# Optimization experiments

Measured on AMD Instinct MI355X. Metric: run time of the kernel, lower is better.

Reference implementation:

```python
import jax, jax.numpy as jnp
import numpy as np

HIDDEN = 2048
HEAD_DIM = 128
NUM_HEADS = 8
NUM_HH = 2          # num_householder
CONV = 4
EPS = 1e-5
KEY_DIM = NUM_HEADS * HEAD_DIM  # 1024


def setup_inputs() -> dict:
    key = jax.random.key(0)
    ks = jax.random.split(key, 14)
    B, L = 2, 512
    s = 0.02
    x = jax.random.normal(ks[0], (B, L, HIDDEN), jnp.float32)
    Wq = jax.random.normal(ks[1], (HIDDEN, KEY_DIM), jnp.float32) * s
    Wk = jax.random.normal(ks[2], (HIDDEN, KEY_DIM * NUM_HH), jnp.float32) * s
    Wv = jax.random.normal(ks[3], (HIDDEN, KEY_DIM * NUM_HH), jnp.float32) * s
    Wb = jax.random.normal(ks[4], (HIDDEN, NUM_HEADS * NUM_HH), jnp.float32) * s
    Wa = jax.random.normal(ks[5], (HIDDEN, NUM_HEADS), jnp.float32) * s
    A_log = jnp.log(jax.random.uniform(ks[6], (NUM_HEADS,), jnp.float32, 1e-3, 16.0))
    dt = jnp.exp(jax.random.uniform(ks[7], (NUM_HEADS,), jnp.float32)
                 * (np.float32(np.log(0.1)) - np.float32(np.log(0.001)))
                 + np.float32(np.log(0.001)))
    dt = jnp.maximum(dt, 1e-4)
    dt_bias = dt + jnp.log(-jnp.expm1(-dt))
    conv_q_w = jax.random.normal(ks[8], (KEY_DIM, 1, CONV), jnp.float32) * 0.1
    conv_k_w = jax.random.normal(ks[9], (KEY_DIM * NUM_HH, 1, CONV), jnp.float32) * 0.1
    conv_v_w = jax.random.normal(ks[10], (KEY_DIM * NUM_HH, 1, CONV), jnp.float32) * 0.1
    Wg = jax.random.normal(ks[11], (HIDDEN, KEY_DIM), jnp.float32) * s
    norm_w = jnp.ones((HEAD_DIM,), jnp.float32)
    Wo = jax.random.normal(ks[12], (KEY_DIM, HIDDEN), jnp.float32) * s
    return dict(x=x, Wq=Wq, Wk=Wk, Wv=Wv, Wb=Wb, Wa=Wa, A_log=A_log,
                dt_bias=dt_bias, conv_q_w=conv_q_w, conv_k_w=conv_k_w,
                conv_v_w=conv_v_w, Wg=Wg, norm_w=norm_w, Wo=Wo)


def _causal_conv_silu(x, w):
    # x: (B, L, C); w: (C, 1, K) depthwise causal conv, then SiLU
    y = jax.lax.conv_general_dilated(
        jnp.swapaxes(x, 1, 2), w, window_strides=(1,),
        padding=[(w.shape[-1] - 1, 0)],
        feature_group_count=w.shape[0],
        dimension_numbers=('NCH', 'OIH', 'NCH'))
    return jnp.swapaxes(jax.nn.silu(y), 1, 2)


def _l2norm(x):
    n = jnp.sqrt(jnp.sum(x * x, axis=-1, keepdims=True))
    return x / jnp.maximum(n, 1e-12)


def reference(x, Wq, Wk, Wv, Wb, Wa, A_log, dt_bias,
              conv_q_w, conv_k_w, conv_v_w, Wg, norm_w, Wo):
    B, L, _ = x.shape
    H, Dh, nh = NUM_HEADS, HEAD_DIM, NUM_HH

    q = _causal_conv_silu(x @ Wq, conv_q_w).reshape(B, L, H, Dh)
    k = _causal_conv_silu(x @ Wk, conv_k_w).reshape(B, L, nh, H, Dh)
    v = _causal_conv_silu(x @ Wv, conv_v_w).reshape(B, L, nh, H, Dh)

    q = _l2norm(q) / np.float32(np.sqrt(Dh))
    k = _l2norm(k)

    beta = 2.0 * jax.nn.sigmoid(x @ Wb).reshape(B, L, nh, H)  # allow_neg_eigval
    g = -jnp.exp(A_log) * jax.nn.softplus(x @ Wa + dt_bias)    # (B, L, H)

    def step(state, inp):
        # state: (B, H, Dh, Dh)
        q_t, k_t, v_t, b_t, g_t = inp  # (B,H,Dh),(B,nh,H,Dh),(B,nh,H,Dh),(B,nh,H),(B,H)
        state = state * jnp.exp(g_t)[..., None, None]  # gate at first sub-step
        for j in range(nh):  # Householder / delta-rule updates
            kj = k_t[:, j]
            corr = jnp.einsum('bhk,bhkv->bhv', kj, state)
            u = (v_t[:, j] - corr) * b_t[:, j][..., None]
            state = state + jnp.einsum('bhk,bhv->bhkv', kj, u)
        o_t = jnp.einsum('bhk,bhkv->bhv', q_t, state)  # readout at last sub-step
        return state, o_t

    state0 = jnp.zeros((B, H, Dh, Dh), x.dtype)
    xs = (jnp.moveaxis(q, 1, 0), jnp.moveaxis(k, 1, 0), jnp.moveaxis(v, 1, 0),
          jnp.moveaxis(beta, 1, 0), jnp.moveaxis(g, 1, 0))
    state, o = jax.lax.scan(step, state0, xs)
    o = jnp.moveaxis(o, 0, 1)  # (B, L, H, Dh)

    # gated RMSNorm: normalize o, scale by weight, gate with silu(g_proj(x))
    gate = (x @ Wg).reshape(B, L, H, Dh)
    o = o * jax.lax.rsqrt(jnp.mean(o * o, axis=-1, keepdims=True) + EPS)
    o = o * norm_w * jax.nn.silu(gate)

    out = o.reshape(B, L, H * Dh) @ Wo
    return out, state
```

## Files before the change

### kernel.cpp

```cpp
#include <hip/hip_runtime.h>
#include <hip/hip_bf16.h>
#include <cmath>

#define B_   2
#define L_   512
#define HID  2048
#define DH   128
#define NH   8
#define NHH  2
#define ROWS 1024
#define NFUSE 6144

typedef float  f32x2  __attribute__((ext_vector_type(2)));
typedef float  f32x4  __attribute__((ext_vector_type(4)));
typedef __bf16 bf16x8 __attribute__((ext_vector_type(8)));

#define AS1(p) ((const __attribute__((address_space(1))) unsigned int*)(p))
#define AS3(p) ((__attribute__((address_space(3))) unsigned int*)(p))

__device__ __forceinline__ float dpp_xor1(float x) {
  int r = __builtin_amdgcn_update_dpp(0, __float_as_int(x), 0xB1, 0xF, 0xF, true);
  return __int_as_float(r);
}
__device__ __forceinline__ float dpp_xor2(float x) {
  int r = __builtin_amdgcn_update_dpp(0, __float_as_int(x), 0x4E, 0xF, 0xF, true);
  return __int_as_float(r);
}
__device__ __forceinline__ float dpp_hmirror(float x) {
  int r = __builtin_amdgcn_update_dpp(0, __float_as_int(x), 0x141, 0xF, 0xF, true);
  return __int_as_float(r);
}
__device__ __forceinline__ float dpp_rmirror(float x) {
  int r = __builtin_amdgcn_update_dpp(0, __float_as_int(x), 0x140, 0xF, 0xF, true);
  return __int_as_float(r);
}

__global__ void f2bf_kernel(const float* __restrict__ in, __hip_bfloat16* __restrict__ out, int n) {
  int i = blockIdx.x * 256 + threadIdx.x;
  if (i < n) out[i] = __float2bfloat16(in[i]);
}

__global__ __launch_bounds__(256) void transpose5_kernel(const float* __restrict__ Wq,
                                                         const float* __restrict__ Wk,
                                                         const float* __restrict__ Wv,
                                                         const float* __restrict__ Wg,
                                                         const float* __restrict__ Wo,
                                                         __hip_bfloat16* __restrict__ WT,
                                                         __hip_bfloat16* __restrict__ WoT) {
  const float* in; __hip_bfloat16* out; int K, N;
  switch (blockIdx.z) {
    case 0: in = Wq; out = WT;                          K = 2048; N = 1024; break;
    case 1: in = Wk; out = WT + (size_t)1024 * 2048;    K = 2048; N = 2048; break;
    case 2: in = Wv; out = WT + (size_t)3072 * 2048;    K = 2048; N = 2048; break;
    case 3: in = Wg; out = WT + (size_t)5120 * 2048;    K = 2048; N = 1024; break;
    default: in = Wo; out = WoT;                        K = 1024; N = 2048; break;
  }
  __shared__ float tile[32][33];
  int n0 = blockIdx.x * 32, k0 = blockIdx.y * 32;
  if (n0 >= N || k0 >= K) return;
  int tx = threadIdx.x, ty = threadIdx.y;
#pragma unroll
  for (int i = 0; i < 32; i += 8)
    tile[ty + i][tx] = in[(size_t)(k0 + ty + i) * N + n0 + tx];
  __syncthreads();
#pragma unroll
  for (int i = 0; i < 32; i += 8)
    out[(size_t)(n0 + ty + i) * K + k0 + tx] = __float2bfloat16(tile[tx][ty + i]);
}

__global__ __launch_bounds__(256) void gemm_bf16(const __hip_bfloat16* __restrict__ A,
                                                 const __hip_bfloat16* __restrict__ BT,
                                                 float* __restrict__ C, int M, int N, int K) {
  __shared__ __align__(16) __hip_bfloat16 lA[128 * 32];
  __shared__ __align__(16) __hip_bfloat16 lB[128 * 32];
  const int tid = threadIdx.x;
  const int lane = tid & 63;
  const int w = tid >> 6;
  const int wr = w >> 1, wc = w & 1;
  const int row0 = blockIdx.y * 128;
  const int col0 = blockIdx.x * 128;
  f32x4 acc[4][4];
#pragma unroll
  for (int m = 0; m < 4; ++m)
#pragma unroll
    for (int n = 0; n < 4; ++n) acc[m][n] = {0.f, 0.f, 0.f, 0.f};
  const int fr = lane & 15;
  const int ko = (lane >> 4) * 8;
  for (int kt = 0; kt < K; kt += 32) {
#pragma unroll
    for (int i = 0; i < 2; ++i) {
      int elem = (w * 2 + i) * 512 + lane * 8;
      int rr = elem >> 5, cc = elem & 31;
      const __hip_bfloat16* srcA = A + (size_t)(row0 + rr) * K + kt + cc;
      __builtin_amdgcn_global_load_lds(AS1(srcA), AS3(&lA[(w * 2 + i) * 512]), 16, 0, 0);
      const __hip_bfloat16* srcB = BT + (size_t)(col0 + rr) * K + kt + cc;
      __builtin_amdgcn_global_load_lds(AS1(srcB), AS3(&lB[(w * 2 + i) * 512]), 16, 0, 0);
    }
    __syncthreads();
    bf16x8 af[4], bfr[4];
#pragma unroll
    for (int m = 0; m < 4; ++m)
      af[m] = *reinterpret_cast<const bf16x8*>(&lA[(wr * 64 + m * 16 + fr) * 32 + ko]);
#pragma unroll
    for (int n = 0; n < 4; ++n)
      bfr[n] = *reinterpret_cast<const bf16x8*>(&lB[(wc * 64 + n * 16 + fr) * 32 + ko]);
#pragma unroll
    for (int m = 0; m < 4; ++m)
#pragma unroll
      for (int n = 0; n < 4; ++n)
        acc[m][n] = __builtin_amdgcn_mfma_f32_16x16x32_bf16(af[m], bfr[n], acc[m][n], 0, 0, 0);
    __syncthreads();
  }
  const int rq = (lane >> 4) * 4;
#pragma unroll
  for (int m = 0; m < 4; ++m)
#pragma unroll
    for (int n = 0; n < 4; ++n)
#pragma unroll
      for (int r = 0; r < 4; ++r)
        C[(size_t)(row0 + wr * 64 + m * 16 + rq + r) * N + (col0 + wc * 64 + n * 16 + fr)] =
            acc[m][n][r];
}

__device__ __forceinline__ float silu_f(float y) { return y / (1.f + __expf(-y)); }

__global__ __launch_bounds__(64) void ba_fused_kernel(const float* __restrict__ x,
                                                      const float* __restrict__ Wb,
                                                      const float* __restrict__ Wa,
                                                      const float* __restrict__ A_log,
                                                      const float* __restrict__ dt_bias,
                                                      float* __restrict__ beta_s,
                                                      float* __restrict__ ge_s) {
  const int row = blockIdx.x;
  const int lane = threadIdx.x;
  f32x4 aB0 = {0,0,0,0}, aB1 = {0,0,0,0}, aB2 = {0,0,0,0}, aB3 = {0,0,0,0};
  f32x4 aA0 = {0,0,0,0}, aA1 = {0,0,0,0};
  const float* xr = x + (size_t)row * HID;
  for (int i = 0; i < 32; ++i) {
    int k = lane + i * 64;
    float xv = xr[k];
    const f32x4* wb4 = (const f32x4*)(Wb + (size_t)k * 16);
    const f32x4* wa4 = (const f32x4*)(Wa + (size_t)k * 8);
    aB0 += wb4[0] * xv; aB1 += wb4[1] * xv; aB2 += wb4[2] * xv; aB3 += wb4[3] * xv;
    aA0 += wa4[0] * xv; aA1 += wa4[1] * xv;
  }
  __shared__ float red[64][25];
#pragma unroll
  for (int c = 0; c < 4; ++c) {
    red[lane][0 + c]  = aB0[c];
    red[lane][4 + c]  = aB1[c];
    red[lane][8 + c]  = aB2[c];
    red[lane][12 + c] = aB3[c];
    red[lane][16 + c] = aA0[c];
    red[lane][20 + c] = aA1[c];
  }
  if (lane < 24) {
    float s = 0.f;
#pragma unroll 8
    for (int i = 0; i < 64; ++i) s += red[i][lane];
    int b = row >> 9, t = row & 511;
    if (lane < 16) {
      int j = lane >> 3, h = lane & 7;
      beta_s[(((size_t)(b * 8 + h)) * 2 + j) * 512 + t] = 2.f / (1.f + __expf(-s));
    } else {
      int h = lane - 16;
      float vv = s + dt_bias[h];
      float sp = (vv > 20.f) ? vv : log1pf(__expf(vv));
      ge_s[((size_t)(b * 8 + h)) * 512 + t] = __expf(-__expf(A_log[h]) * sp);
    }
  }
}

__global__ __launch_bounds__(128) void conv_qkv_kernel(const float* __restrict__ qkvg,
                                                       const float* __restrict__ wq,
                                                       const float* __restrict__ wk,
                                                       const float* __restrict__ wv,
                                                       float* __restrict__ q_s,
                                                       float* __restrict__ k_s,
                                                       float* __restrict__ v_s) {
  int bt = blockIdx.x;
  int yy = blockIdx.y;
  int d  = threadIdx.x;
  int b = bt >> 9, t = bt & 511;
  __shared__ float red[2];
  if (yy < 8) {
    int h = yy, c = h * 128 + d;
    float y = 0.f;
#pragma unroll
    for (int tau = 0; tau < 4; ++tau) {
      int tt = t - 3 + tau;
      float xv = (tt >= 0) ? qkvg[(size_t)(b * 512 + tt) * NFUSE + c] : 0.f;
      y += xv * wq[c * 4 + tau];
    }
    y = silu_f(y);
    float ss = y * y;
#pragma unroll
    for (int off = 32; off; off >>= 1) ss += __shfl_down(ss, off);
    if ((d & 63) == 0) red[d >> 6] = ss;
    __syncthreads();
    float scale = (1.f / fmaxf(sqrtf(red[0] + red[1]), 1e-12f)) * 0.08838834764831845f;
    q_s[((size_t)(b * 8 + h) * 512 + t) * 128 + d] = y * scale;
  } else if (yy < 24) {
    int jh = yy - 8;
    int j = jh >> 3, h = jh & 7;
    int c = j * 1024 + h * 128 + d;
    float y = 0.f;
#pragma unroll
    for (int tau = 0; tau < 4; ++tau) {
      int tt = t - 3 + tau;
      float xv = (tt >= 0) ? qkvg[(size_t)(b * 512 + tt) * NFUSE + 1024 + c] : 0.f;
      y += xv * wk[c * 4 + tau];
    }
    y = silu_f(y);
    float ss = y * y;
#pragma unroll
    for (int off = 32; off; off >>= 1) ss += __shfl_down(ss, off);
    if ((d & 63) == 0) red[d >> 6] = ss;
    __syncthreads();
    float scale = 1.f / fmaxf(sqrtf(red[0] + red[1]), 1e-12f);
    k_s[(((size_t)(b * 8 + h) * 2 + j) * 512 + t) * 128 + d] = y * scale;
  } else {
    int jh = yy - 24;
    int j = jh >> 3, h = jh & 7;
    int c = j * 1024 + h * 128 + d;
    float y = 0.f;
#pragma unroll
    for (int tau = 0; tau < 4; ++tau) {
      int tt = t - 3 + tau;
      float xv = (tt >= 0) ? qkvg[(size_t)(b * 512 + tt) * NFUSE + 3072 + c] : 0.f;
      y += xv * wv[c * 4 + tau];
    }
    v_s[(((size_t)(b * 8 + h) * 2 + j) * 512 + t) * 128 + d] = silu_f(y);
  }
}

__global__ __launch_bounds__(64) void dots_kernel(const float* __restrict__ q_s,
                                                  const float* __restrict__ k_s,
                                                  float* __restrict__ dots_s) {
  const int bh = blockIdx.x;
  const int ty = blockIdx.y;
  const int lane = threadIdx.x;
  const int e  = lane & 7;
  const int tl = lane >> 3;
  const int t = ty * 8 + tl;
  const float* k0 = k_s + ((size_t)bh * 2 + 0) * 512 * 128 + (size_t)t * 128 + e * 16;
  const float* k1 = k_s + ((size_t)bh * 2 + 1) * 512 * 128 + (size_t)t * 128 + e * 16;
  const float* qq = q_s + (size_t)bh * 512 * 128 + (size_t)t * 128 + e * 16;
  float d01 = 0.f, dq0 = 0.f, dq1 = 0.f;
#pragma unroll
  for (int i = 0; i < 4; ++i) {
    f32x4 a = *(const f32x4*)(k0 + i * 4);
    f32x4 b = *(const f32x4*)(k1 + i * 4);
    f32x4 c = *(const f32x4*)(qq + i * 4);
    f32x4 t1 = a * b, t2 = c * a, t3 = c * b;
    d01 += (t1[0] + t1[1]) + (t1[2] + t1[3]);
    dq0 += (t2[0] + t2[1]) + (t2[2] + t2[3]);
    dq1 += (t3[0] + t3[1]) + (t3[2] + t3[3]);
  }
  d01 += dpp_xor1(d01); d01 += dpp_xor2(d01); d01 += dpp_hmirror(d01);
  dq0 += dpp_xor1(dq0); dq0 += dpp_xor2(dq0); dq0 += dpp_hmirror(dq0);
  dq1 += dpp_xor1(dq1); dq1 += dpp_xor2(dq1); dq1 += dpp_hmirror(dq1);
  if (e == 0) {
    float* dst = dots_s + (size_t)bh * 3 * 512;
    dst[0 * 512 + t] = d01;
    dst[1 * 512 + t] = dq0;
    dst[2 * 512 + t] = dq1;
  }
}

#define R4(X) X(0) X(1) X(2) X(3)
#define CH 12
#define TSTEP 8
#define STEPF (3 * 16 * CH)
#define TILEF (TSTEP * STEPF)

__global__ __launch_bounds__(64, 1) void scan_kernel(const float* __restrict__ q_s,
                                                     const float* __restrict__ k_s,
                                                     const float* __restrict__ v_s,
                                                     const float* __restrict__ beta_s,
                                                     const float* __restrict__ ge_s,
                                                     const float* __restrict__ dots_s,
                                                     float* __restrict__ o_s,
                                                     float* __restrict__ state_out) {
  const int blk = blockIdx.x;
  const int bh  = blk >> 5;
  const int wg  = blk & 31;
  const int lane = threadIdx.x;
  const int kr = lane & 15;
  const int vi = lane >> 4;
  const int v  = wg * 4 + vi;

  __shared__ __align__(16) float lds[2][TILEF];
  __shared__ __align__(16) float vbuf[2][2][TSTEP][4];
  __shared__ __align__(16) float lds_bg[6][512];

  f32x4 s0 = {0.f, 0.f, 0.f, 0.f}, s1 = {0.f, 0.f, 0.f, 0.f};
#define DECLG(j) f32x4 Gk0_##j, Gk1_##j, Gq_##j;
  R4(DECLG)
#undef DECLG
  float Gv;
#define DECLSET(S) f32x4 S##_a0, S##_a1, S##_b0, S##_b1, S##_c0, S##_c1; \
  float S##_eg, S##_bb0, S##_bb1, S##_d01, S##_dq0, S##_dq1, S##_mv0, S##_mv1;
  DECLSET(A) DECLSET(B)
#undef DECLSET

  const float* g_k0 = k_s + ((size_t)bh * 2 + 0) * 512 * 128;
  const float* g_k1 = k_s + ((size_t)bh * 2 + 1) * 512 * 128;
  const float* g_q  = q_s + (size_t)bh * 512 * 128;
  const float* g_v0w = v_s + ((size_t)bh * 2 + 0) * 512 * 128 + wg * 4;
  const float* g_v1w = v_s + ((size_t)bh * 2 + 1) * 512 * 128 + wg * 4;
  const float* b0p = beta_s + ((size_t)bh * 2 + 0) * 512;
  const float* b1p = beta_s + ((size_t)bh * 2 + 1) * 512;
  const float* gp  = ge_s + (size_t)bh * 512;
  const float* dp  = dots_s + (size_t)bh * 3 * 512;

#pragma unroll
  for (int i = 0; i < 2; ++i) {
    int c4 = lane + i * 64;
    *(f32x4*)&lds_bg[0][c4 * 4] = *(const f32x4*)(gp  + c4 * 4);
    *(f32x4*)&lds_bg[1][c4 * 4] = *(const f32x4*)(b0p + c4 * 4);
    *(f32x4*)&lds_bg[2][c4 * 4] = *(const f32x4*)(b1p + c4 * 4);
    *(f32x4*)&lds_bg[3][c4 * 4] = *(const f32x4*)(dp + 0 * 512 + c4 * 4);
    *(f32x4*)&lds_bg[4][c4 * 4] = *(const f32x4*)(dp + 1 * 512 + c4 * 4);
    *(f32x4*)&lds_bg[5][c4 * 4] = *(const f32x4*)(dp + 2 * 512 + c4 * 4);
  }

  const int vhalf = lane >> 5;
  const int vli = lane & 31;
  const int vtl = vli >> 2, vc = vli & 3;
  const float* vsrc = vhalf ? g_v1w : g_v0w;

#define LD1(j) { Gk0_##j = p0[lane + j * 64]; Gk1_##j = p1[lane + j * 64]; Gq_##j = pq[lane + j * 64]; }
#define LOAD_G(T) { const f32x4* __restrict__ p0 = (const f32x4*)(g_k0 + (size_t)(T) * 1024); \
                    const f32x4* __restrict__ p1 = (const f32x4*)(g_k1 + (size_t)(T) * 1024); \
                    const f32x4* __restrict__ pq = (const f32x4*)(g_q  + (size_t)(T) * 1024); \
                    R4(LD1) }
#define LOAD_V(T) { Gv = vsrc[(size_t)(T) * 1024 + vtl * 128 + vc]; }
#define WR1(j) { int g_ = lane + 64 * j; int tl_ = g_ >> 5; int kr_ = (g_ & 31) >> 1; \
                 int c_ = 4 * (g_ & 1); \
    *(f32x4*)&lds[bsel][((tl_ * 3 + 0) * 16 + kr_) * CH + c_] = Gk0_##j; \
    *(f32x4*)&lds[bsel][((tl_ * 3 + 1) * 16 + kr_) * CH + c_] = Gk1_##j; \
    *(f32x4*)&lds[bsel][((tl_ * 3 + 2) * 16 + kr_) * CH + c_] = Gq_##j; }
#define WRITE_G(b) { const int bsel = (b); R4(WR1) }
#define WRITE_V(b) { vbuf[b][vhalf][vtl][vc] = Gv; }

#define LOAD_SET(S, bufx, tlx, tg) { \
    const f32x4* __restrict__ pk0 = (const f32x4*)&lds[bufx][(((tlx) * 3 + 0) * 16 + kr) * CH]; \
    const f32x4* __restrict__ pk1 = (const f32x4*)&lds[bufx][(((tlx) * 3 + 1) * 16 + kr) * CH]; \
    const f32x4* __restrict__ pqq = (const f32x4*)&lds[bufx][(((tlx) * 3 + 2) * 16 + kr) * CH]; \
    S##_a0 = pk0[0]; S##_a1 = pk0[1]; \
    S##_b0 = pk1[0]; S##_b1 = pk1[1]; \
    S##_c0 = pqq[0]; S##_c1 = pqq[1]; \
    S##_eg  = lds_bg[0][tg]; S##_bb0 = lds_bg[1][tg]; S##_bb1 = lds_bg[2][tg]; \
    S##_d01 = lds_bg[3][tg]; S##_dq0 = lds_bg[4][tg]; S##_dq1 = lds_bg[5][tg]; \
    S##_mv0 = vbuf[bufx][0][tlx][vi]; S##_mv1 = vbuf[bufx][1][tlx][vi]; } \
    __builtin_amdgcn_sched_barrier(0);

#define COMPUTE(S, tt) { \
    s0 *= S##_eg; s1 *= S##_eg; \
    f32x4 r0v = S##_a0 * s0; r0v += S##_a1 * s1; \
    f32x4 r1v = S##_b0 * s0; r1v += S##_b1 * s1; \
    f32x4 rqv = S##_c0 * s0; rqv += S##_c1 * s1; \
    float p0 = (r0v[0] + r0v[1]) + (r0v[2] + r0v[3]); \
    float p1 = (r1v[0] + r1v[1]) + (r1v[2] + r1v[3]); \
    float pq2 = (rqv[0] + rqv[1]) + (rqv[2] + rqv[3]); \
    p0 += dpp_xor1(p0);    p1 += dpp_xor1(p1);    pq2 += dpp_xor1(pq2); \
    p0 += dpp_xor2(p0);    p1 += dpp_xor2(p1);    pq2 += dpp_xor2(pq2); \
    p0 += dpp_hmirror(p0); p1 += dpp_hmirror(p1); pq2 += dpp_hmirror(pq2); \
    p0 += dpp_rmirror(p0); p1 += dpp_rmirror(p1); pq2 += dpp_rmirror(pq2); \
    const float u0 = (S##_mv0 - p0) * S##_bb0; \
    const float u1 = (S##_mv1 - p1 - S##_d01 * u0) * S##_bb1; \
    const float oo = pq2 + S##_dq0 * u0 + S##_dq1 * u1; \
    s0 += S##_a0 * u0; s1 += S##_a1 * u0; \
    s0 += S##_b0 * u1; s1 += S##_b1 * u1; \
    if (kr == 0) o_s[((size_t)bh * 512 + (tt)) * 128 + v] = oo; }

  LOAD_G(0) LOAD_V(0)
  WRITE_G(0) WRITE_V(0)
  LOAD_G(1) LOAD_V(1)
  LOAD_SET(A, 0, 0, 0)

  for (int T = 0; T < 64; ++T) {
    const int buf = T & 1;
    if (T < 63) { WRITE_G(buf ^ 1) WRITE_V(buf ^ 1) }
    if (T < 62) { LOAD_G(T + 2) LOAD_V(T + 2) }
    const int t0 = T * 8;
    LOAD_SET(B, buf, 1, t0 + 1)                  COMPUTE(A, t0 + 0)
    LOAD_SET(A, buf, 2, t0 + 2)                  COMPUTE(B, t0 + 1)
    LOAD_SET(B, buf, 3, t0 + 3)                  COMPUTE(A, t0 + 2)
    LOAD_SET(A, buf, 4, t0 + 4)                  COMPUTE(B, t0 + 3)
    LOAD_SET(B, buf, 5, t0 + 5)                  COMPUTE(A, t0 + 4)
    LOAD_SET(A, buf, 6, t0 + 6)                  COMPUTE(B, t0 + 5)
    LOAD_SET(B, buf, 7, t0 + 7)                  COMPUTE(A, t0 + 6)
    LOAD_SET(A, buf ^ 1, 0, (t0 + 8) & 511)     COMPUTE(B, t0 + 7)
  }

  float* base = state_out + (size_t)bh * 128 * 128 + v;
#pragma unroll
  for (int i = 0; i < 4; ++i) {
    base[(kr * 8 + i) * 128]     = s0[i];
    base[(kr * 8 + 4 + i) * 128] = s1[i];
  }
}

__global__ __launch_bounds__(128) void post_kernel(const float* __restrict__ o_s,
                                                   const float* __restrict__ qkvg,
                                                   const float* __restrict__ norm_w,
                                                   __hip_bfloat16* __restrict__ Afin) {
  int bt = blockIdx.x;
  int h = blockIdx.y;
  int d = threadIdx.x;
  int b = bt >> 9, t = bt & 511;
  int bh = b * 8 + h;
  float o = o_s[((size_t)bh * 512 + t) * 128 + d];
  __shared__ float red[2];
  float ss = o * o;
#pragma unroll
  for (int off = 32; off; off >>= 1) ss += __shfl_down(ss, off);
  if ((d & 63) == 0) red[d >> 6] = ss;
  __syncthreads();
  float mean = (red[0] + red[1]) * (1.f / 128.f);
  float r = rsqrtf(mean + 1e-5f);
  float gate = qkvg[(size_t)bt * NFUSE + 5120 + h * 128 + d];
  float val = o * r * norm_w[d] * silu_f(gate);
  Afin[(size_t)bt * 1024 + h * 128 + d] = __float2bfloat16(val);
}

extern "C" void kernel_launch(void* const* d_in, const int* in_sizes, int n_in,
                              void* d_out, int out_size, void* d_ws, size_t ws_size,
                              hipStream_t stream) {
  const float* x       = (const float*)d_in[0];
  const float* Wq      = (const float*)d_in[1];
  const float* Wk      = (const float*)d_in[2];
  const float* Wv      = (const float*)d_in[3];
  const float* Wb      = (const float*)d_in[4];
  const float* Wa      = (const float*)d_in[5];
  const float* A_log   = (const float*)d_in[6];
  const float* dt_bias = (const float*)d_in[7];
  const float* cqw     = (const float*)d_in[8];
  const float* ckw     = (const float*)d_in[9];
  const float* cvw     = (const float*)d_in[10];
  const float* Wg      = (const float*)d_in[11];
  const float* norm_w  = (const float*)d_in[12];
  const float* Wo      = (const float*)d_in[13];

  char* ws = (char*)d_ws;
  size_t off = 0;
  auto alloc = [&](size_t bytes) {
    void* p = ws + off;
    off += (bytes + 255) & ~(size_t)255;
    return p;
  };
  __hip_bfloat16* xbf  = (__hip_bfloat16*)alloc((size_t)2097152 * 2);
  __hip_bfloat16* WT   = (__hip_bfloat16*)alloc((size_t)NFUSE * 2048 * 2);
  __hip_bfloat16* WoT  = (__hip_bfloat16*)alloc((size_t)2097152 * 2);
  float* qkvg   = (float*)alloc((size_t)ROWS * NFUSE * 4);
  float* q_s    = (float*)alloc((size_t)1048576 * 4);
  float* k_s    = (float*)alloc((size_t)2097152 * 4);
  float* v_s    = (float*)alloc((size_t)2097152 * 4);
  float* beta_s = (float*)alloc((size_t)16384 * 4);
  float* ge_s   = (float*)alloc((size_t)8192 * 4);
  float* dots_s = (float*)alloc((size_t)16 * 3 * 512 * 4);
  float* o_s    = (float*)alloc((size_t)1048576 * 4);
  __hip_bfloat16* Afin = (__hip_bfloat16*)alloc((size_t)1048576 * 2);

  float* out_main  = (float*)d_out;
  float* out_state = out_main + 2097152;

  dim3 tb(32, 8);
  f2bf_kernel<<<8192, 256, 0, stream>>>(x, xbf, 2097152);
  transpose5_kernel<<<dim3(64, 64, 5), tb, 0, stream>>>(Wq, Wk, Wv, Wg, Wo, WT, WoT);

  gemm_bf16<<<dim3(48, 8), 256, 0, stream>>>(xbf, WT, qkvg, 1024, NFUSE, 2048);
  ba_fused_kernel<<<1024, 64, 0, stream>>>(x, Wb, Wa, A_log, dt_bias, beta_s, ge_s);

  conv_qkv_kernel<<<dim3(1024, 40), 128, 0, stream>>>(qkvg, cqw, ckw, cvw, q_s, k_s, v_s);
  dots_kernel<<<dim3(16, 64), 64, 0, stream>>>(q_s, k_s, dots_s);

  scan_kernel<<<512, 64, 0, stream>>>(q_s, k_s, v_s, beta_s, ge_s, dots_s, o_s, out_state);

  post_kernel<<<dim3(1024, 8), 128, 0, stream>>>(o_s, qkvg, norm_w, Afin);
  gemm_bf16<<<dim3(16, 8), 256, 0, stream>>>(Afin, WoT, out_main, 1024, 2048, 1024);
}
```

Before: 256.0 us.

## Process two timesteps per scan iteration using precomputed cross-step key dot products

```diff
diff --git a/kernel.cpp b/kernel.cpp
--- a/kernel.cpp
+++ b/kernel.cpp
@@ -238,33 +238,41 @@
                                                   const float* __restrict__ k_s,
                                                   float* __restrict__ dots_s) {
   const int bh = blockIdx.x;
-  const int ty = blockIdx.y;
+  const int py = blockIdx.y;
   const int lane = threadIdx.x;
   const int e  = lane & 7;
-  const int tl = lane >> 3;
-  const int t = ty * 8 + tl;
-  const float* k0 = k_s + ((size_t)bh * 2 + 0) * 512 * 128 + (size_t)t * 128 + e * 16;
-  const float* k1 = k_s + ((size_t)bh * 2 + 1) * 512 * 128 + (size_t)t * 128 + e * 16;
-  const float* qq = q_s + (size_t)bh * 512 * 128 + (size_t)t * 128 + e * 16;
-  float d01 = 0.f, dq0 = 0.f, dq1 = 0.f;
+  const int pl = lane >> 3;
+  const int p = py * 8 + pl;
+  const int tA = 2 * p;
+  const float* k0A = k_s + ((size_t)bh * 2 + 0) * 512 * 128 + (size_t)tA * 128 + e * 16;
+  const float* k1A = k_s + ((size_t)bh * 2 + 1) * 512 * 128 + (size_t)tA * 128 + e * 16;
+  const float* qA  = q_s + (size_t)bh * 512 * 128 + (size_t)tA * 128 + e * 16;
+  float d0=0,d1=0,d2=0,d3=0,d4=0,d5=0,d6=0,d7=0,d8=0,d9=0,d10=0,d11=0;
 #pragma unroll
   for (int i = 0; i < 4; ++i) {
-    f32x4 a = *(const f32x4*)(k0 + i * 4);
-    f32x4 b = *(const f32x4*)(k1 + i * 4);
-    f32x4 c = *(const f32x4*)(qq + i * 4);
-    f32x4 t1 = a * b, t2 = c * a, t3 = c * b;
-    d01 += (t1[0] + t1[1]) + (t1[2] + t1[3]);
-    dq0 += (t2[0] + t2[1]) + (t2[2] + t2[3]);
-    dq1 += (t3[0] + t3[1]) + (t3[2] + t3[3]);
-  }
-  d01 += dpp_xor1(d01); d01 += dpp_xor2(d01); d01 += dpp_hmirror(d01);
-  dq0 += dpp_xor1(dq0); dq0 += dpp_xor2(dq0); dq0 += dpp_hmirror(dq0);
-  dq1 += dpp_xor1(dq1); dq1 += dpp_xor2(dq1); dq1 += dpp_hmirror(dq1);
+    f32x4 a0 = *(const f32x4*)(k0A + i * 4);
+    f32x4 a1 = *(const f32x4*)(k1A + i * 4);
+    f32x4 qa = *(const f32x4*)(qA  + i * 4);
+    f32x4 b0 = *(const f32x4*)(k0A + 128 + i * 4);
+    f32x4 b1 = *(const f32x4*)(k1A + 128 + i * 4);
+    f32x4 qb = *(const f32x4*)(qA  + 128 + i * 4);
+    f32x4 t;
+#define HS(acc, u, w) t = (u) * (w); acc += (t[0] + t[1]) + (t[2] + t[3]);
+    HS(d0, a1, a0) HS(d1, qa, a0) HS(d2, qa, a1)
+    HS(d3, b1, b0) HS(d4, qb, b0) HS(d5, qb, b1)
+    HS(d6, b0, a0) HS(d7, b0, a1) HS(d8, b1, a0) HS(d9, b1, a1)
+    HS(d10, qb, a0) HS(d11, qb, a1)
+#undef HS
+  }
+#define RED(dd) dd += dpp_xor1(dd); dd += dpp_xor2(dd); dd += dpp_hmirror(dd);
+  RED(d0) RED(d1) RED(d2) RED(d3) RED(d4) RED(d5)
+  RED(d6) RED(d7) RED(d8) RED(d9) RED(d10) RED(d11)
+#undef RED
   if (e == 0) {
-    float* dst = dots_s + (size_t)bh * 3 * 512;
-    dst[0 * 512 + t] = d01;
-    dst[1 * 512 + t] = dq0;
-    dst[2 * 512 + t] = dq1;
+    float* dst = dots_s + (size_t)bh * 12 * 256 + p;
+    dst[0*256]=d0; dst[1*256]=d1; dst[2*256]=d2;  dst[3*256]=d3;
+    dst[4*256]=d4; dst[5*256]=d5; dst[6*256]=d6;  dst[7*256]=d7;
+    dst[8*256]=d8; dst[9*256]=d9; dst[10*256]=d10; dst[11*256]=d11;
   }
 }
 
@@ -292,15 +300,19 @@
 
   __shared__ __align__(16) float lds[2][TILEF];
   __shared__ __align__(16) float vbuf[2][2][TSTEP][4];
-  __shared__ __align__(16) float lds_bg[6][512];
+  __shared__ __align__(16) float lds_sc[256][20];
 
   f32x4 s0 = {0.f, 0.f, 0.f, 0.f}, s1 = {0.f, 0.f, 0.f, 0.f};
 #define DECLG(j) f32x4 Gk0_##j, Gk1_##j, Gq_##j;
   R4(DECLG)
 #undef DECLG
   float Gv;
-#define DECLSET(S) f32x4 S##_a0, S##_a1, S##_b0, S##_b1, S##_c0, S##_c1; \
-  float S##_eg, S##_bb0, S##_bb1, S##_d01, S##_dq0, S##_dq1, S##_mv0, S##_mv1;
+#define DECLSET(S) f32x4 S##_a0A,S##_a1A,S##_b0A,S##_b1A,S##_c0A,S##_c1A, \
+                         S##_a0B,S##_a1B,S##_b0B,S##_b1B,S##_c0B,S##_c1B; \
+  float S##_gA,S##_gB,S##_bb0A,S##_bb1A,S##_bb0B,S##_bb1B, \
+        S##_d01A,S##_dq0A,S##_dq1A,S##_d01B,S##_dq0B,S##_dq1B, \
+        S##_c00,S##_c01,S##_c10,S##_c11,S##_cq0,S##_cq1, \
+        S##_mv0A,S##_mv1A,S##_mv0B,S##_mv1B;
   DECLSET(A) DECLSET(B)
 #undef DECLSET
 
@@ -312,17 +324,17 @@
   const float* b0p = beta_s + ((size_t)bh * 2 + 0) * 512;
   const float* b1p = beta_s + ((size_t)bh * 2 + 1) * 512;
   const float* gp  = ge_s + (size_t)bh * 512;
-  const float* dp  = dots_s + (size_t)bh * 3 * 512;
-
-#pragma unroll
-  for (int i = 0; i < 2; ++i) {
-    int c4 = lane + i * 64;
-    *(f32x4*)&lds_bg[0][c4 * 4] = *(const f32x4*)(gp  + c4 * 4);
-    *(f32x4*)&lds_bg[1][c4 * 4] = *(const f32x4*)(b0p + c4 * 4);
-    *(f32x4*)&lds_bg[2][c4 * 4] = *(const f32x4*)(b1p + c4 * 4);
-    *(f32x4*)&lds_bg[3][c4 * 4] = *(const f32x4*)(dp + 0 * 512 + c4 * 4);
-    *(f32x4*)&lds_bg[4][c4 * 4] = *(const f32x4*)(dp + 1 * 512 + c4 * 4);
-    *(f32x4*)&lds_bg[5][c4 * 4] = *(const f32x4*)(dp + 2 * 512 + c4 * 4);
+  const float* dp  = dots_s + (size_t)bh * 12 * 256;
+
+#pragma unroll
+  for (int i = 0; i < 4; ++i) {
+    int p = lane + i * 64;
+    int tA = 2 * p;
+    lds_sc[p][0] = gp[tA];      lds_sc[p][1] = gp[tA + 1];
+    lds_sc[p][2] = b0p[tA];     lds_sc[p][3] = b1p[tA];
+    lds_sc[p][4] = b0p[tA + 1]; lds_sc[p][5] = b1p[tA + 1];
+#pragma unroll
+    for (int j = 0; j < 12; ++j) lds_sc[p][6 + j] = dp[j * 256 + p];
   }
 
   const int vhalf = lane >> 5;
@@ -344,55 +356,81 @@
 #define WRITE_G(b) { const int bsel = (b); R4(WR1) }
 #define WRITE_V(b) { vbuf[b][vhalf][vtl][vc] = Gv; }
 
-#define LOAD_SET(S, bufx, tlx, tg) { \
-    const f32x4* __restrict__ pk0 = (const f32x4*)&lds[bufx][(((tlx) * 3 + 0) * 16 + kr) * CH]; \
-    const f32x4* __restrict__ pk1 = (const f32x4*)&lds[bufx][(((tlx) * 3 + 1) * 16 + kr) * CH]; \
-    const f32x4* __restrict__ pqq = (const f32x4*)&lds[bufx][(((tlx) * 3 + 2) * 16 + kr) * CH]; \
-    S##_a0 = pk0[0]; S##_a1 = pk0[1]; \
-    S##_b0 = pk1[0]; S##_b1 = pk1[1]; \
-    S##_c0 = pqq[0]; S##_c1 = pqq[1]; \
-    S##_eg  = lds_bg[0][tg]; S##_bb0 = lds_bg[1][tg]; S##_bb1 = lds_bg[2][tg]; \
-    S##_d01 = lds_bg[3][tg]; S##_dq0 = lds_bg[4][tg]; S##_dq1 = lds_bg[5][tg]; \
-    S##_mv0 = vbuf[bufx][0][tlx][vi]; S##_mv1 = vbuf[bufx][1][tlx][vi]; } \
+#define LOAD_PAIR(S, bufx, tlx, pg) { \
+    const f32x4* pk0A_ = (const f32x4*)&lds[bufx][(((tlx) * 3 + 0) * 16 + kr) * CH]; \
+    const f32x4* pk1A_ = (const f32x4*)&lds[bufx][(((tlx) * 3 + 1) * 16 + kr) * CH]; \
+    const f32x4* pqA_  = (const f32x4*)&lds[bufx][(((tlx) * 3 + 2) * 16 + kr) * CH]; \
+    const f32x4* pk0B_ = (const f32x4*)&lds[bufx][((((tlx) + 1) * 3 + 0) * 16 + kr) * CH]; \
+    const f32x4* pk1B_ = (const f32x4*)&lds[bufx][((((tlx) + 1) * 3 + 1) * 16 + kr) * CH]; \
+    const f32x4* pqB_  = (const f32x4*)&lds[bufx][((((tlx) + 1) * 3 + 2) * 16 + kr) * CH]; \
+    S##_a0A = pk0A_[0]; S##_a1A = pk0A_[1]; \
+    S##_b0A = pk1A_[0]; S##_b1A = pk1A_[1]; \
+    S##_c0A = pqA_[0];  S##_c1A = pqA_[1]; \
+    S##_a0B = pk0B_[0]; S##_a1B = pk0B_[1]; \
+    S##_b0B = pk1B_[0]; S##_b1B = pk1B_[1]; \
+    S##_c0B = pqB_[0];  S##_c1B = pqB_[1]; \
+    const f32x4* sc_ = (const f32x4*)&lds_sc[(pg) & 255][0]; \
+    f32x4 y0_ = sc_[0], y1_ = sc_[1], y2_ = sc_[2], y3_ = sc_[3], y4_ = sc_[4]; \
+    S##_gA = y0_[0]; S##_gB = y0_[1]; S##_bb0A = y0_[2]; S##_bb1A = y0_[3]; \
+    S##_bb0B = y1_[0]; S##_bb1B = y1_[1]; S##_d01A = y1_[2]; S##_dq0A = y1_[3]; \
+    S##_dq1A = y2_[0]; S##_d01B = y2_[1]; S##_dq0B = y2_[2]; S##_dq1B = y2_[3]; \
+    S##_c00 = y3_[0]; S##_c01 = y3_[1]; S##_c10 = y3_[2]; S##_c11 = y3_[3]; \
+    S##_cq0 = y4_[0]; S##_cq1 = y4_[1]; \
+    S##_mv0A = vbuf[bufx][0][tlx][vi]; S##_mv1A = vbuf[bufx][1][tlx][vi]; \
+    S##_mv0B = vbuf[bufx][0][(tlx) + 1][vi]; S##_mv1B = vbuf[bufx][1][(tlx) + 1][vi]; } \
     __builtin_amdgcn_sched_barrier(0);
 
-#define COMPUTE(S, tt) { \
-    s0 *= S##_eg; s1 *= S##_eg; \
-    f32x4 r0v = S##_a0 * s0; r0v += S##_a1 * s1; \
-    f32x4 r1v = S##_b0 * s0; r1v += S##_b1 * s1; \
-    f32x4 rqv = S##_c0 * s0; rqv += S##_c1 * s1; \
-    float p0 = (r0v[0] + r0v[1]) + (r0v[2] + r0v[3]); \
-    float p1 = (r1v[0] + r1v[1]) + (r1v[2] + r1v[3]); \
-    float pq2 = (rqv[0] + rqv[1]) + (rqv[2] + rqv[3]); \
-    p0 += dpp_xor1(p0);    p1 += dpp_xor1(p1);    pq2 += dpp_xor1(pq2); \
-    p0 += dpp_xor2(p0);    p1 += dpp_xor2(p1);    pq2 += dpp_xor2(pq2); \
-    p0 += dpp_hmirror(p0); p1 += dpp_hmirror(p1); pq2 += dpp_hmirror(pq2); \
-    p0 += dpp_rmirror(p0); p1 += dpp_rmirror(p1); pq2 += dpp_rmirror(pq2); \
-    const float u0 = (S##_mv0 - p0) * S##_bb0; \
-    const float u1 = (S##_mv1 - p1 - S##_d01 * u0) * S##_bb1; \
-    const float oo = pq2 + S##_dq0 * u0 + S##_dq1 * u1; \
-    s0 += S##_a0 * u0; s1 += S##_a1 * u0; \
-    s0 += S##_b0 * u1; s1 += S##_b1 * u1; \
-    if (kr == 0) o_s[((size_t)bh * 512 + (tt)) * 128 + v] = oo; }
+#define COMPUTE_PAIR(S, pg) { \
+    f32x4 r0A_ = S##_a0A * s0; r0A_ += S##_a1A * s1; \
+    f32x4 r1A_ = S##_b0A * s0; r1A_ += S##_b1A * s1; \
+    f32x4 rqA_ = S##_c0A * s0; rqA_ += S##_c1A * s1; \
+    f32x4 r0B_ = S##_a0B * s0; r0B_ += S##_a1B * s1; \
+    f32x4 r1B_ = S##_b0B * s0; r1B_ += S##_b1B * s1; \
+    f32x4 rqB_ = S##_c0B * s0; rqB_ += S##_c1B * s1; \
+    float h0A = (r0A_[0] + r0A_[1]) + (r0A_[2] + r0A_[3]); \
+    float h1A = (r1A_[0] + r1A_[1]) + (r1A_[2] + r1A_[3]); \
+    float hqA = (rqA_[0] + rqA_[1]) + (rqA_[2] + rqA_[3]); \
+    float h0B = (r0B_[0] + r0B_[1]) + (r0B_[2] + r0B_[3]); \
+    float h1B = (r1B_[0] + r1B_[1]) + (r1B_[2] + r1B_[3]); \
+    float hqB = (rqB_[0] + rqB_[1]) + (rqB_[2] + rqB_[3]); \
+    h0A += dpp_xor1(h0A); h1A += dpp_xor1(h1A); hqA += dpp_xor1(hqA); \
+    h0B += dpp_xor1(h0B); h1B += dpp_xor1(h1B); hqB += dpp_xor1(hqB); \
+    h0A += dpp_xor2(h0A); h1A += dpp_xor2(h1A); hqA += dpp_xor2(hqA); \
+    h0B += dpp_xor2(h0B); h1B += dpp_xor2(h1B); hqB += dpp_xor2(hqB); \
+    h0A += dpp_hmirror(h0A); h1A += dpp_hmirror(h1A); hqA += dpp_hmirror(hqA); \
+    h0B += dpp_hmirror(h0B); h1B += dpp_hmirror(h1B); hqB += dpp_hmirror(hqB); \
+    h0A += dpp_rmirror(h0A); h1A += dpp_rmirror(h1A); hqA += dpp_rmirror(hqA); \
+    h0B += dpp_rmirror(h0B); h1B += dpp_rmirror(h1B); hqB += dpp_rmirror(hqB); \
+    const float u0A_ = (S##_mv0A - S##_gA * h0A) * S##_bb0A; \
+    const float u1A_ = (S##_mv1A - S##_gA * h1A - S##_d01A * u0A_) * S##_bb1A; \
+    const float u0B_ = (S##_mv0B - S##_gB * (S##_gA * h0B + S##_c00 * u0A_ + S##_c01 * u1A_)) * S##_bb0B; \
+    const float u1B_ = (S##_mv1B - S##_gB * (S##_gA * h1B + S##_c10 * u0A_ + S##_c11 * u1A_) \
+                        - S##_d01B * u0B_) * S##_bb1B; \
+    const float oA_ = S##_gA * hqA + S##_dq0A * u0A_ + S##_dq1A * u1A_; \
+    const float oB_ = S##_gB * (S##_gA * hqB + S##_cq0 * u0A_ + S##_cq1 * u1A_) \
+                      + S##_dq0B * u0B_ + S##_dq1B * u1B_; \
+    const float gg_ = S##_gA * S##_gB; \
+    const float w0_ = S##_gB * u0A_, w1_ = S##_gB * u1A_; \
+    s0 *= gg_; s0 += S##_a0A * w0_; s0 += S##_b0A * w1_; s0 += S##_a0B * u0B_; s0 += S##_b0B * u1B_; \
+    s1 *= gg_; s1 += S##_a1A * w0_; s1 += S##_b1A * w1_; s1 += S##_a1B * u0B_; s1 += S##_b1B * u1B_; \
+    if (kr == 0) { const int tA_ = 2 * (pg); \
+      o_s[((size_t)bh * 512 + tA_) * 128 + v] = oA_; \
+      o_s[((size_t)bh * 512 + tA_ + 1) * 128 + v] = oB_; } }
 
   LOAD_G(0) LOAD_V(0)
   WRITE_G(0) WRITE_V(0)
   LOAD_G(1) LOAD_V(1)
-  LOAD_SET(A, 0, 0, 0)
+  LOAD_PAIR(A, 0, 0, 0)
 
   for (int T = 0; T < 64; ++T) {
     const int buf = T & 1;
     if (T < 63) { WRITE_G(buf ^ 1) WRITE_V(buf ^ 1) }
     if (T < 62) { LOAD_G(T + 2) LOAD_V(T + 2) }
-    const int t0 = T * 8;
-    LOAD_SET(B, buf, 1, t0 + 1)                  COMPUTE(A, t0 + 0)
-    LOAD_SET(A, buf, 2, t0 + 2)                  COMPUTE(B, t0 + 1)
-    LOAD_SET(B, buf, 3, t0 + 3)                  COMPUTE(A, t0 + 2)
-    LOAD_SET(A, buf, 4, t0 + 4)                  COMPUTE(B, t0 + 3)
-    LOAD_SET(B, buf, 5, t0 + 5)                  COMPUTE(A, t0 + 4)
-    LOAD_SET(A, buf, 6, t0 + 6)                  COMPUTE(B, t0 + 5)
-    LOAD_SET(B, buf, 7, t0 + 7)                  COMPUTE(A, t0 + 6)
-    LOAD_SET(A, buf ^ 1, 0, (t0 + 8) & 511)     COMPUTE(B, t0 + 7)
+    const int p0i = T * 4;
+    LOAD_PAIR(B, buf, 2, p0i + 1)              COMPUTE_PAIR(A, p0i + 0)
+    LOAD_PAIR(A, buf, 4, p0i + 2)              COMPUTE_PAIR(B, p0i + 1)
+    LOAD_PAIR(B, buf, 6, p0i + 3)              COMPUTE_PAIR(A, p0i + 2)
+    LOAD_PAIR(A, buf ^ 1, 0, (p0i + 4) & 255)  COMPUTE_PAIR(B, p0i + 3)
   }
 
   float* base = state_out + (size_t)bh * 128 * 128 + v;
@@ -460,7 +498,7 @@
   float* v_s    = (float*)alloc((size_t)2097152 * 4);
   float* beta_s = (float*)alloc((size_t)16384 * 4);
   float* ge_s   = (float*)alloc((size_t)8192 * 4);
-  float* dots_s = (float*)alloc((size_t)16 * 3 * 512 * 4);
+  float* dots_s = (float*)alloc((size_t)16 * 12 * 256 * 4);
   float* o_s    = (float*)alloc((size_t)1048576 * 4);
   __hip_bfloat16* Afin = (__hip_bfloat16*)alloc((size_t)1048576 * 2);
 
@@ -475,7 +513,7 @@
   ba_fused_kernel<<<1024, 64, 0, stream>>>(x, Wb, Wa, A_log, dt_bias, beta_s, ge_s);
 
   conv_qkv_kernel<<<dim3(1024, 40), 128, 0, stream>>>(qkvg, cqw, ckw, cvw, q_s, k_s, v_s);
-  dots_kernel<<<dim3(16, 64), 64, 0, stream>>>(q_s, k_s, dots_s);
+  dots_kernel<<<dim3(16, 32), 64, 0, stream>>>(q_s, k_s, dots_s);
 
   scan_kernel<<<512, 64, 0, stream>>>(q_s, k_s, v_s, beta_s, ge_s, dots_s, o_s, out_state);
 
```

Result: no change. 251.2 us (-1.9%).
